# Kernel optimization log

Hardware: AMD Instinct MI355X
Metric: run time of the kernel (lower is better)

The kernel has to match this reference:

```python
import jax, jax.numpy as jnp
import numpy as np

MAX_KLEN = 11  # kernel lengths drawn from {7, 9, 11}


def setup_inputs() -> dict:
    B, T, K = 32, 512, 4096
    rng = np.random.default_rng(0)
    # kernel lengths ~ uniform over {7, 9, 11}
    klen = np.array([7, 9, 11])[rng.integers(0, 3, size=K)]
    tap_mask = (np.arange(MAX_KLEN)[None, :] < klen[:, None])
    # weights: N(0,1), mean-centered over the actual taps, zero-padded to MAX_KLEN
    w = rng.standard_normal((K, MAX_KLEN)).astype(np.float32) * tap_mask
    w = w - (w.sum(1, keepdims=True) / klen[:, None]).astype(np.float32) * tap_mask
    # bias ~ U[-1, 1)
    bias = (rng.random(K) * 2 - 1).astype(np.float32)
    # dilation = floor(2**s), s ~ U[0, ln(T-1) - ln(klen-1)]
    A = np.log(T - 1) - np.log(klen - 1)
    dil = np.floor(2.0 ** (rng.random(K) * A)).astype(np.int64)
    # padding = dil*(klen-1)/2 with prob 1/2, else 0  (klen-1 is even -> exact)
    pad = (dil * (klen - 1) // 2) * rng.integers(0, 2, size=K)
    # torch conv1d output length
    out_len = T + 2 * pad - dil * (klen - 1)
    x = jax.random.normal(jax.random.key(0), (B, T), dtype=jnp.float32)
    return {
        'x': x,
        'weight': jnp.asarray(w),
        'bias': jnp.asarray(bias),
        'dilation': jnp.asarray(dil, jnp.int32),
        'padding': jnp.asarray(pad, jnp.int32),
        'out_len': jnp.asarray(out_len, jnp.int32),
    }


def reference(x, weight, bias, dilation, padding, out_len):
    # x: [B, T]; weight: [K, MAX_KLEN] zero-padded; bias/dilation/padding/out_len: [K]
    B, T = x.shape
    K = weight.shape[0]
    P = T  # padding <= dil*(klen-1)/2  =>  out_len <= T
    p = jnp.arange(P, dtype=jnp.int32)
    acc = jnp.zeros((B, K, P), dtype=x.dtype)
    # fixed small loop over taps; all kernels processed at once per tap
    for j in range(MAX_KLEN):
        idx = p[None, :] - padding[:, None] + j * dilation[:, None]  # [K, P]
        ok = (idx >= 0) & (idx < T)
        xg = x[:, jnp.clip(idx, 0, T - 1)]  # [B, K, P]
        acc = acc + (weight[:, j][:, None] * ok.astype(x.dtype)) * xg
    conv = acc + bias[None, :, None]  # [B, K, P]
    valid = (p[None, :] < out_len[:, None])  # [K, P]
    neg_inf = jnp.asarray(-jnp.inf, dtype=x.dtype)
    mx = jnp.max(jnp.where(valid[None], conv, neg_inf), axis=-1)  # [B, K]
    ppv = jnp.sum(((conv > 0) & valid[None]).astype(x.dtype), axis=-1) / out_len.astype(x.dtype)
    # einops 'b s f -> b (s f)': interleave (max_k, ppv_k) per kernel
    feats = jnp.stack([mx, ppv], axis=-1).reshape(B, 2 * K)
    return feats
```

## Files before the change

kernel.cpp:

```cpp
#include <hip/hip_runtime.h>
#include <hip/hip_fp16.h>

#define TLEN 512
#define KLEN 11
#define XPAD 256
#define XTOT 1024
#define NEGINF2 0xFC00FC00u

__device__ __forceinline__ unsigned pkmax_u(unsigned a, unsigned b) {
    unsigned d;
    asm("v_pk_max_f16 %0, %1, %2" : "=v"(d) : "v"(a), "v"(b));
    return d;
}
__device__ __forceinline__ unsigned pkadd_u(unsigned a, unsigned b) {
    unsigned d;
    asm("v_pk_add_f16 %0, %1, %2" : "=v"(d) : "v"(a), "v"(b));
    return d;
}
__device__ __forceinline__ void pkfma_s(unsigned& acc, unsigned w2s, unsigned h) {
    asm("v_pk_fma_f16 %0, %1, %2, %0" : "+v"(acc) : "s"(w2s), "v"(h));
}

__device__ __forceinline__ unsigned wred_pkmax(unsigned x) {
    unsigned t;
    t = __builtin_amdgcn_update_dpp((int)NEGINF2, (int)x, 0x111, 0xF, 0xF, false);
    x = pkmax_u(x, t);
    t = __builtin_amdgcn_update_dpp((int)NEGINF2, (int)x, 0x112, 0xF, 0xF, false);
    x = pkmax_u(x, t);
    t = __builtin_amdgcn_update_dpp((int)NEGINF2, (int)x, 0x114, 0xF, 0xF, false);
    x = pkmax_u(x, t);
    t = __builtin_amdgcn_update_dpp((int)NEGINF2, (int)x, 0x118, 0xF, 0xF, false);
    x = pkmax_u(x, t);
    t = __builtin_amdgcn_update_dpp((int)NEGINF2, (int)x, 0x142, 0xA, 0xF, false);
    x = pkmax_u(x, t);
    t = __builtin_amdgcn_update_dpp((int)NEGINF2, (int)x, 0x143, 0xC, 0xF, false);
    x = pkmax_u(x, t);
    return (unsigned)__builtin_amdgcn_readlane((int)x, 63);
}
__device__ __forceinline__ unsigned wred_pkadd(unsigned x) {
    unsigned t;
    t = __builtin_amdgcn_update_dpp(0, (int)x, 0x111, 0xF, 0xF, false);
    x = pkadd_u(x, t);
    t = __builtin_amdgcn_update_dpp(0, (int)x, 0x112, 0xF, 0xF, false);
    x = pkadd_u(x, t);
    t = __builtin_amdgcn_update_dpp(0, (int)x, 0x114, 0xF, 0xF, false);
    x = pkadd_u(x, t);
    t = __builtin_amdgcn_update_dpp(0, (int)x, 0x118, 0xF, 0xF, false);
    x = pkadd_u(x, t);
    t = __builtin_amdgcn_update_dpp(0, (int)x, 0x142, 0xA, 0xF, false);
    x = pkadd_u(x, t);
    t = __builtin_amdgcn_update_dpp(0, (int)x, 0x143, 0xC, 0xF, false);
    x = pkadd_u(x, t);
    return (unsigned)__builtin_amdgcn_readlane((int)x, 63);
}

__device__ __forceinline__ __half2 as_h2(unsigned u) {
    __half2 h; __builtin_memcpy(&h, &u, 4); return h;
}
__device__ __forceinline__ unsigned as_u(__half2 h) {
    unsigned u; __builtin_memcpy(&u, &h, 4); return u;
}

__global__ __launch_bounds__(256, 8) void rf_fused(
    const float* __restrict__ x, const float* __restrict__ weight,
    const float* __restrict__ bias, const int* __restrict__ dilation,
    const int* __restrict__ padding, const int* __restrict__ out_len,
    float* __restrict__ out, int K)
{
    __shared__ uint4 xs[XTOT];
    const int t = threadIdx.x;

    const uint4 z = make_uint4(0u, 0u, 0u, 0u);
    xs[t] = z;
    xs[768 + t] = z;
    const float* xg = x + (size_t)blockIdx.y * 8 * TLEN;
    #pragma unroll
    for (int half_ = 0; half_ < 2; ++half_) {
        const int pos = t + half_ * 256;
        float v[8];
        #pragma unroll
        for (int q = 0; q < 8; ++q) v[q] = xg[q * TLEN + pos];
        uint4 s;
        s.x = as_u(__floats2half2_rn(v[0], v[1]));
        s.y = as_u(__floats2half2_rn(v[2], v[3]));
        s.z = as_u(__floats2half2_rn(v[4], v[5]));
        s.w = as_u(__floats2half2_rn(v[6], v[7]));
        xs[XPAD + pos] = s;
    }
    __syncthreads();

    const int lane = t & 63;
    const int ks = __builtin_amdgcn_readfirstlane(blockIdx.x * 4 + (t >> 6));

    const int dil  = dilation[ks];
    const int pd   = padding[ks];
    const int olen = out_len[ks];
    unsigned w2s[KLEN];
    bool wnz[KLEN];
    #pragma unroll
    for (int j = 0; j < KLEN; ++j) {
        const float wv = weight[ks * KLEN + j];
        wnz[j] = (wv != 0.0f);
        w2s[j] = __builtin_amdgcn_readfirstlane((int)as_u(__float2half2_rn(wv)));
    }
    const unsigned bias2 = __builtin_amdgcn_readfirstlane(
        (int)as_u(__float2half2_rn(bias[ks])));
    const __half2 zero2 = __float2half2_rn(0.0f);

    const int vbase = XPAD + lane - pd;

    unsigned acc[8][4];
    #pragma unroll
    for (int c = 0; c < 8; ++c)
        #pragma unroll
        for (int q = 0; q < 4; ++q) acc[c][q] = bias2;

    #pragma unroll
    for (int j = 0; j < KLEN; ++j) {
        if (wnz[j]) {
            const uint4* xp = xs + (vbase + j * dil);
            #pragma unroll
            for (int c = 0; c < 8; ++c) {
                if (c * 64 < olen) {
                    const uint4 r = xp[c * 64];
                    pkfma_s(acc[c][0], w2s[j], r.x);
                    pkfma_s(acc[c][1], w2s[j], r.y);
                    pkfma_s(acc[c][2], w2s[j], r.z);
                    pkfma_s(acc[c][3], w2s[j], r.w);
                }
            }
        }
    }

    unsigned mxu[4], cfu[4];
    #pragma unroll
    for (int q = 0; q < 4; ++q) { mxu[q] = NEGINF2; cfu[q] = 0u; }

    #pragma unroll
    for (int c = 0; c < 8; ++c) {
        const int p0 = c * 64;
        if (p0 + 64 <= olen) {
            #pragma unroll
            for (int q = 0; q < 4; ++q) {
                mxu[q] = pkmax_u(mxu[q], acc[c][q]);
                cfu[q] = pkadd_u(cfu[q], as_u(__hgt2(as_h2(acc[c][q]), zero2)));
            }
        } else if (p0 < olen) {
            const bool vld = lane < (olen - p0);
            #pragma unroll
            for (int q = 0; q < 4; ++q) {
                mxu[q] = pkmax_u(mxu[q], vld ? acc[c][q] : NEGINF2);
                const unsigned g = vld ? as_u(__hgt2(as_h2(acc[c][q]), zero2)) : 0u;
                cfu[q] = pkadd_u(cfu[q], g);
            }
        }
    }

    #pragma unroll
    for (int q = 0; q < 4; ++q) {
        mxu[q] = wred_pkmax(mxu[q]);
        cfu[q] = wred_pkadd(cfu[q]);
    }

    if (lane == 0) {
        const float inv = 1.0f / (float)olen;
        const size_t row = (size_t)2 * K;
        float* o = out + (size_t)blockIdx.y * 8 * row + 2 * ks;
        #pragma unroll
        for (int q = 0; q < 4; ++q) {
            const __half2 m = as_h2(mxu[q]);
            const __half2 c = as_h2(cfu[q]);
            *(float2*)(o + (2 * q) * row)     = make_float2(__low2float(m),  __low2float(c) * inv);
            *(float2*)(o + (2 * q + 1) * row) = make_float2(__high2float(m), __high2float(c) * inv);
        }
    }
}

extern "C" void kernel_launch(void* const* d_in, const int* in_sizes, int n_in,
                              void* d_out, int out_size, void* d_ws, size_t ws_size,
                              hipStream_t stream) {
    const float* x    = (const float*)d_in[0];
    const float* w    = (const float*)d_in[1];
    const float* bias = (const float*)d_in[2];
    const int* dil    = (const int*)d_in[3];
    const int* pad    = (const int*)d_in[4];
    const int* olen   = (const int*)d_in[5];
    float* out        = (float*)d_out;

    const int K = in_sizes[2];
    const int B = in_sizes[0] / TLEN;

    dim3 grid(K / 4, B / 8);
    rf_fused<<<grid, 256, 0, stream>>>(x, w, bias, dil, pad, olen, out, K);
    (void)n_in; (void)out_size; (void)d_ws; (void)ws_size;
}
```

Before: 90.78 us.

## Split each kernel's output positions across two waves with LDS merge

Doubles the block to 512 threads so each kernel's 512 output positions are handled by two waves, 256 positions each, instead of one wave covering all 8 chunks. The partial max and positive-count values are merged through shared memory after an extra pair of barriers. The intent is more parallelism and latency hiding, with half the accumulator registers per thread. In exchange it adds duplicated per-wave weight loads, two extra __syncthreads, and a higher thread count per block. Workload balance may also suffer when out_len is short, because the upper-half waves then idle.

```diff
diff --git a/kernel.cpp b/kernel.cpp
--- a/kernel.cpp
+++ b/kernel.cpp
@@ -61,7 +61,7 @@
     unsigned u; __builtin_memcpy(&u, &h, 4); return u;
 }
 
-__global__ __launch_bounds__(256, 8) void rf_fused(
+__global__ __launch_bounds__(512, 8) void rf_split(
     const float* __restrict__ x, const float* __restrict__ weight,
     const float* __restrict__ bias, const int* __restrict__ dilation,
     const int* __restrict__ padding, const int* __restrict__ out_len,
@@ -70,13 +70,11 @@
     __shared__ uint4 xs[XTOT];
     const int t = threadIdx.x;
 
-    const uint4 z = make_uint4(0u, 0u, 0u, 0u);
-    xs[t] = z;
-    xs[768 + t] = z;
-    const float* xg = x + (size_t)blockIdx.y * 8 * TLEN;
-    #pragma unroll
-    for (int half_ = 0; half_ < 2; ++half_) {
-        const int pos = t + half_ * 256;
+    if (t < 256) xs[t] = make_uint4(0u, 0u, 0u, 0u);
+    else         xs[512 + t] = make_uint4(0u, 0u, 0u, 0u);
+    {
+        const float* xg = x + (size_t)blockIdx.y * 8 * TLEN;
+        const int pos = t;
         float v[8];
         #pragma unroll
         for (int q = 0; q < 8; ++q) v[q] = xg[q * TLEN + pos];
@@ -89,8 +87,10 @@
     }
     __syncthreads();
 
+    const int wave = t >> 6;
     const int lane = t & 63;
-    const int ks = __builtin_amdgcn_readfirstlane(blockIdx.x * 4 + (t >> 6));
+    const int half_ = wave >> 2;
+    const int ks = __builtin_amdgcn_readfirstlane(blockIdx.x * 4 + (wave & 3));
 
     const int dil  = dilation[ks];
     const int pd   = padding[ks];
@@ -107,11 +107,11 @@
         (int)as_u(__float2half2_rn(bias[ks])));
     const __half2 zero2 = __float2half2_rn(0.0f);
 
-    const int vbase = XPAD + lane - pd;
-
-    unsigned acc[8][4];
-    #pragma unroll
-    for (int c = 0; c < 8; ++c)
+    const int vbase = XPAD + half_ * 256 + lane - pd;
+
+    unsigned acc[4][4];
+    #pragma unroll
+    for (int c = 0; c < 4; ++c)
         #pragma unroll
         for (int q = 0; q < 4; ++q) acc[c][q] = bias2;
 
@@ -120,8 +120,8 @@
         if (wnz[j]) {
             const uint4* xp = xs + (vbase + j * dil);
             #pragma unroll
-            for (int c = 0; c < 8; ++c) {
-                if (c * 64 < olen) {
+            for (int c = 0; c < 4; ++c) {
+                if ((half_ * 4 + c) * 64 < olen) {
                     const uint4 r = xp[c * 64];
                     pkfma_s(acc[c][0], w2s[j], r.x);
                     pkfma_s(acc[c][1], w2s[j], r.y);
@@ -137,8 +137,8 @@
     for (int q = 0; q < 4; ++q) { mxu[q] = NEGINF2; cfu[q] = 0u; }
 
     #pragma unroll
-    for (int c = 0; c < 8; ++c) {
-        const int p0 = c * 64;
+    for (int c = 0; c < 4; ++c) {
+        const int p0 = (half_ * 4 + c) * 64;
         if (p0 + 64 <= olen) {
             #pragma unroll
             for (int q = 0; q < 4; ++q) {
@@ -162,7 +162,20 @@
         cfu[q] = wred_pkadd(cfu[q]);
     }
 
-    if (lane == 0) {
+    __syncthreads();
+    if (half_ == 1 && lane == 0) {
+        xs[(wave - 4) * 2]     = make_uint4(mxu[0], mxu[1], mxu[2], mxu[3]);
+        xs[(wave - 4) * 2 + 1] = make_uint4(cfu[0], cfu[1], cfu[2], cfu[3]);
+    }
+    __syncthreads();
+    if (half_ == 0 && lane == 0) {
+        const uint4 pm = xs[wave * 2];
+        const uint4 pc = xs[wave * 2 + 1];
+        mxu[0] = pkmax_u(mxu[0], pm.x); mxu[1] = pkmax_u(mxu[1], pm.y);
+        mxu[2] = pkmax_u(mxu[2], pm.z); mxu[3] = pkmax_u(mxu[3], pm.w);
+        cfu[0] = pkadd_u(cfu[0], pc.x); cfu[1] = pkadd_u(cfu[1], pc.y);
+        cfu[2] = pkadd_u(cfu[2], pc.z); cfu[3] = pkadd_u(cfu[3], pc.w);
+
         const float inv = 1.0f / (float)olen;
         const size_t row = (size_t)2 * K;
         float* o = out + (size_t)blockIdx.y * 8 * row + 2 * ks;
@@ -191,6 +204,6 @@
     const int B = in_sizes[0] / TLEN;
 
     dim3 grid(K / 4, B / 8);
-    rf_fused<<<grid, 256, 0, stream>>>(x, w, bias, dil, pad, olen, out, K);
+    rf_split<<<grid, 512, 0, stream>>>(x, w, bias, dil, pad, olen, out, K);
     (void)n_in; (void)out_size; (void)d_ws; (void)ws_size;
 }
```

After: 100.0 us. +10.2%, slower.

## Interchange tap and chunk loops to accumulate per chunk and reduce immediately

Applied to the files above, without the earlier changes.

The loops are reordered so each 64-position chunk loads all taps from LDS, runs its packed FMAs into four accumulators, and folds the result into the max and positive-count reductions before moving on. This replaces the 8x4 accumulator array held across all taps with a small live set, cutting register pressure so the 8-waves-per-SIMD occupancy target can be met without spills. In exchange, up to 11 uint4 LDS loads per chunk are live at once, and the branch on the weight being nonzero is now evaluated per chunk.

```diff
diff --git a/kernel.cpp b/kernel.cpp
--- a/kernel.cpp
+++ b/kernel.cpp
@@ -61,7 +61,7 @@
     unsigned u; __builtin_memcpy(&u, &h, 4); return u;
 }
 
-__global__ __launch_bounds__(256, 8) void rf_fused(
+__global__ __launch_bounds__(256, 8) void rf_co(
     const float* __restrict__ x, const float* __restrict__ weight,
     const float* __restrict__ bias, const int* __restrict__ dilation,
     const int* __restrict__ padding, const int* __restrict__ out_len,
@@ -75,8 +75,8 @@
     xs[768 + t] = z;
     const float* xg = x + (size_t)blockIdx.y * 8 * TLEN;
     #pragma unroll
-    for (int half_ = 0; half_ < 2; ++half_) {
-        const int pos = t + half_ * 256;
+    for (int h = 0; h < 2; ++h) {
+        const int pos = t + h * 256;
         float v[8];
         #pragma unroll
         for (int q = 0; q < 8; ++q) v[q] = xg[q * TLEN + pos];
@@ -108,29 +108,9 @@
     const __half2 zero2 = __float2half2_rn(0.0f);
 
     const int vbase = XPAD + lane - pd;
-
-    unsigned acc[8][4];
+    int off[KLEN];
     #pragma unroll
-    for (int c = 0; c < 8; ++c)
-        #pragma unroll
-        for (int q = 0; q < 4; ++q) acc[c][q] = bias2;
-
-    #pragma unroll
-    for (int j = 0; j < KLEN; ++j) {
-        if (wnz[j]) {
-            const uint4* xp = xs + (vbase + j * dil);
-            #pragma unroll
-            for (int c = 0; c < 8; ++c) {
-                if (c * 64 < olen) {
-                    const uint4 r = xp[c * 64];
-                    pkfma_s(acc[c][0], w2s[j], r.x);
-                    pkfma_s(acc[c][1], w2s[j], r.y);
-                    pkfma_s(acc[c][2], w2s[j], r.z);
-                    pkfma_s(acc[c][3], w2s[j], r.w);
-                }
-            }
-        }
-    }
+    for (int j = 0; j < KLEN; ++j) off[j] = vbase + j * dil;
 
     unsigned mxu[4], cfu[4];
     #pragma unroll
@@ -139,19 +119,40 @@
     #pragma unroll
     for (int c = 0; c < 8; ++c) {
         const int p0 = c * 64;
-        if (p0 + 64 <= olen) {
+        if (p0 < olen) {
+            uint4 r[KLEN];
             #pragma unroll
-            for (int q = 0; q < 4; ++q) {
-                mxu[q] = pkmax_u(mxu[q], acc[c][q]);
-                cfu[q] = pkadd_u(cfu[q], as_u(__hgt2(as_h2(acc[c][q]), zero2)));
+            for (int j = 0; j < KLEN; ++j)
+                if (wnz[j]) r[j] = xs[off[j] + p0];
+            unsigned a0 = bias2, a1 = bias2, a2 = bias2, a3 = bias2;
+            #pragma unroll
+            for (int j = 0; j < KLEN; ++j) {
+                if (wnz[j]) {
+                    pkfma_s(a0, w2s[j], r[j].x);
+                    pkfma_s(a1, w2s[j], r[j].y);
+                    pkfma_s(a2, w2s[j], r[j].z);
+                    pkfma_s(a3, w2s[j], r[j].w);
+                }
             }
-        } else if (p0 < olen) {
-            const bool vld = lane < (olen - p0);
-            #pragma unroll
-            for (int q = 0; q < 4; ++q) {
-                mxu[q] = pkmax_u(mxu[q], vld ? acc[c][q] : NEGINF2);
-                const unsigned g = vld ? as_u(__hgt2(as_h2(acc[c][q]), zero2)) : 0u;
-                cfu[q] = pkadd_u(cfu[q], g);
+            if (p0 + 64 <= olen) {
+                mxu[0] = pkmax_u(mxu[0], a0);
+                mxu[1] = pkmax_u(mxu[1], a1);
+                mxu[2] = pkmax_u(mxu[2], a2);
+                mxu[3] = pkmax_u(mxu[3], a3);
+                cfu[0] = pkadd_u(cfu[0], as_u(__hgt2(as_h2(a0), zero2)));
+                cfu[1] = pkadd_u(cfu[1], as_u(__hgt2(as_h2(a1), zero2)));
+                cfu[2] = pkadd_u(cfu[2], as_u(__hgt2(as_h2(a2), zero2)));
+                cfu[3] = pkadd_u(cfu[3], as_u(__hgt2(as_h2(a3), zero2)));
+            } else {
+                const bool vld = lane < (olen - p0);
+                mxu[0] = pkmax_u(mxu[0], vld ? a0 : NEGINF2);
+                mxu[1] = pkmax_u(mxu[1], vld ? a1 : NEGINF2);
+                mxu[2] = pkmax_u(mxu[2], vld ? a2 : NEGINF2);
+                mxu[3] = pkmax_u(mxu[3], vld ? a3 : NEGINF2);
+                cfu[0] = pkadd_u(cfu[0], vld ? as_u(__hgt2(as_h2(a0), zero2)) : 0u);
+                cfu[1] = pkadd_u(cfu[1], vld ? as_u(__hgt2(as_h2(a1), zero2)) : 0u);
+                cfu[2] = pkadd_u(cfu[2], vld ? as_u(__hgt2(as_h2(a2), zero2)) : 0u);
+                cfu[3] = pkadd_u(cfu[3], vld ? as_u(__hgt2(as_h2(a3), zero2)) : 0u);
             }
         }
     }
@@ -191,6 +192,6 @@
     const int B = in_sizes[0] / TLEN;
 
     dim3 grid(K / 4, B / 8);
-    rf_fused<<<grid, 256, 0, stream>>>(x, w, bias, dil, pad, olen, out, K);
+    rf_co<<<grid, 256, 0, stream>>>(x, w, bias, dil, pad, olen, out, K);
     (void)n_in; (void)out_size; (void)d_ws; (void)ws_size;
 }
```

After: 102.1 us. +12.5%, slower.
